# Kernel tuning notes

Hardware: AMD Instinct MI355X
Metric: run time of the kernel (lower is better)

## Reference

```python
import jax, jax.numpy as jnp
import numpy as np

PIANO_SAMPLES = 2_621_440          # multiple of 256 (~119 s @ 22050 Hz)
BLOCK = 512
HOP = 256
N_STEPS = PIANO_SAMPLES // HOP      # 10240 loop iterations
N_FRAMES = PIANO_SAMPLES // HOP + 2 # 10242
UPSAMPLE = 256 // 32                # 8, as in F.upsample(scale_factor=8)


def _hamming(n=BLOCK):
    # torch.hamming_window default: periodic=True
    return (0.54 - 0.46 * jnp.cos(2.0 * jnp.pi * jnp.arange(n, dtype=jnp.float32) / n)).astype(jnp.float32)


def _upsample_linear(v, scale):
    # F.upsample(mode='linear', align_corners=False) on a 1D signal
    n = v.shape[0]
    coords = (jnp.arange(n * scale, dtype=jnp.float32) + 0.5) / scale - 0.5
    coords = jnp.clip(coords, 0.0, n - 1.0)
    lo = jnp.floor(coords).astype(jnp.int32)
    hi = jnp.minimum(lo + 1, n - 1)
    w = coords - lo.astype(jnp.float32)
    return v[lo] * (1.0 - w) + v[hi] * w


def setup_inputs() -> dict:
    key = jax.random.key(0)
    k1, k2, k3, k4, k5, k6 = jax.random.split(key, 6)
    return {
        "x": jnp.zeros((1,), jnp.float32),  # unused by the original forward
        "excitation_env": jax.random.uniform(k1, (N_FRAMES * 32,), jnp.float32) * 0.01,
        "tf_real": jax.random.uniform(k2, (N_FRAMES, 257), jnp.float32) * 0.2,
        "tf_imag": jax.random.uniform(k3, (N_FRAMES, 257), jnp.float32) * 0.2,
        "etf_real": jax.random.uniform(k4, (257,), jnp.float32) * 0.2,
        "etf_imag": jax.random.uniform(k5, (257,), jnp.float32) * 0.2,
        # per-step uniform(-1,1) noise (torch draws this inside forward)
        "noise": jax.random.uniform(k6, (N_STEPS, BLOCK), jnp.float32) * 2.0 - 1.0,
    }


def reference(x, excitation_env, tf_real, tf_imag, etf_real, etf_imag, noise):
    tf = (tf_real + 1j * tf_imag).astype(jnp.complex64)      # [N_FRAMES, 257]
    etf = (etf_real + 1j * etf_imag).astype(jnp.complex64)   # [257]
    win = _hamming()

    # excitation envelope: square then linear-upsample x8 -> len PIANO_SAMPLES + 512
    exc = _upsample_linear(excitation_env ** 2, UPSAMPLE)

    # gather all 512-sample excitation windows at hop 256 -> [N_STEPS, 512]
    idx = jnp.arange(N_STEPS)[:, None] * HOP + jnp.arange(BLOCK)[None, :]
    exc_blocks = exc[idx]

    # batched excitation filtering (independent per step -> fully vectorized)
    imp = noise * exc_blocks
    imp = jnp.fft.irfft(jnp.fft.rfft(imp, norm='ortho') * etf, norm='ortho').astype(jnp.float32)

    # impulse added to the *previous* block at steps 1..N_STEPS-1; last block gets none
    imp_next = jnp.concatenate([imp[1:], jnp.zeros((1, BLOCK), imp.dtype)], axis=0)

    def step(s, inp):
        tf_i, inext = inp
        b = win * jnp.fft.irfft(jnp.fft.rfft(s, norm='ortho') * tf_i, norm='ortho').astype(jnp.float32)
        s_next = b + inext
        return s_next, s_next

    s0 = imp[0]  # learned_impulse=False -> first block is the filtered excitation
    _, ys = jax.lax.scan(step, s0, (tf[:N_STEPS], imp_next))

    blocks = jnp.concatenate([s0[None, :], ys], axis=0)  # [N_STEPS+1, 512]

    # overlap-add with hop 256
    n_b = blocks.shape[0]
    out = jnp.zeros((n_b * HOP + (BLOCK - HOP),), blocks.dtype)
    oa_idx = jnp.arange(n_b)[:, None] * HOP + jnp.arange(BLOCK)[None, :]
    out = out.at[oa_idx].add(blocks)
    return out[:PIANO_SAMPLES]
```

## Files before the change

kernel.cpp:

```cpp
#include <hip/hip_runtime.h>
#include <math.h>

#define N_STEPS 10240
#define ROWF2 264
#define ROWF  (ROWF2*2)
#define ENV_N 327744
#define LCH 16
#define KWARM 16

typedef float f4 __attribute__((ext_vector_type(4)));

__device__ inline float2 mkf2(float x, float y) { return make_float2(x, y); }

template<int DIR>
__device__ inline void waveFFT256(float2 v[4], const int l,
                                  const float Tc, const float Ts,
                                  const float ux, const float uy) {
  const int rb = (int)(__brev((unsigned)l) >> 26);
  #pragma unroll
  for (int r = 0; r < 4; ++r) {
    v[r].x = __shfl(v[r].x, rb);
    v[r].y = __shfl(v[r].y, rb);
  }
  #pragma unroll
  for (int s = 0; s < 6; ++s) {
    const int half = 1 << s;
    float wx, wy;
    if (s == 0) { wx = (l & 1) ? -1.f : 1.f; wy = 0.f; }
    else {
      const int idx = (l << (5 - s)) & 63;
      wx = __shfl(Tc, idx);
      float tsv = __shfl(Ts, idx);
      wy = (DIR < 0) ? tsv : -tsv;
    }
    #pragma unroll
    for (int r = 0; r < 4; ++r) {
      float tx = __shfl_xor(v[r].x, half);
      float ty = __shfl_xor(v[r].y, half);
      const bool low = (l & half) == 0;
      float ax = low ? v[r].x : tx, ay = low ? v[r].y : ty;
      float bx = low ? tx : v[r].x, by = low ? ty : v[r].y;
      v[r].x = ax + (wx * bx - wy * by);
      v[r].y = ay + (wx * by + wy * bx);
    }
  }
  const float u2x = ux * ux - uy * uy, u2y = 2.f * ux * uy;
  const float u3x = u2x * ux - u2y * uy, u3y = u2x * uy + u2y * ux;
  float2 t0 = v[0];
  float2 t1 = mkf2(v[1].x * ux - v[1].y * uy, v[1].x * uy + v[1].y * ux);
  float2 t2 = mkf2(v[2].x * u2x - v[2].y * u2y, v[2].x * u2y + v[2].y * u2x);
  float2 t3 = mkf2(v[3].x * u3x - v[3].y * u3y, v[3].x * u3y + v[3].y * u3x);
  float2 p02 = mkf2(t0.x + t2.x, t0.y + t2.y), m02 = mkf2(t0.x - t2.x, t0.y - t2.y);
  float2 p13 = mkf2(t1.x + t3.x, t1.y + t3.y), m13 = mkf2(t1.x - t3.x, t1.y - t3.y);
  v[0] = mkf2(p02.x + p13.x, p02.y + p13.y);
  v[2] = mkf2(p02.x - p13.x, p02.y - p13.y);
  if (DIR < 0) {
    v[1] = mkf2(m02.x + m13.y, m02.y - m13.x);
    v[3] = mkf2(m02.x - m13.y, m02.y + m13.x);
  } else {
    v[1] = mkf2(m02.x - m13.y, m02.y + m13.x);
    v[3] = mkf2(m02.x + m13.y, m02.y - m13.x);
  }
}

__global__ __launch_bounds__(256) void kernA(const float* __restrict__ env,
                                             const float* __restrict__ noise,
                                             const float* __restrict__ tf_re,
                                             const float* __restrict__ etf_re,
                                             const float* __restrict__ etf_im,
                                             float* __restrict__ IMP,
                                             float* __restrict__ T256,
                                             float* __restrict__ I256) {
  const int l = threadIdx.x & 63;
  const int j = blockIdx.x * 4 + (threadIdx.x >> 6);
  float* rowf = IMP + (size_t)j * ROWF;
  float2* row = (float2*)rowf;
  if (j >= N_STEPS) {
    if (j == N_STEPS) {
      #pragma unroll
      for (int r = 0; r < 4; ++r) row[64 * r + l] = mkf2(0.f, 0.f);
      if (l == 0) { row[256] = mkf2(0.f, 0.f); I256[N_STEPS] = 0.f; }
    }
    return;
  }
  const int K = 32 * j + l;
  float e0 = env[K];                e0 *= e0;
  float em = env[max(K - 1, 0)];    em *= em;
  float ep = env[min(K + 1, ENV_N - 1)]; ep *= ep;
  float sm[8];
  #pragma unroll
  for (int u = 0; u < 8; ++u) {
    float val;
    if (u < 4) {
      float fr = 0.5625f + 0.125f * (float)u;
      val = em * (1.f - fr) + e0 * fr;
      if (K == 0) val = e0;
    } else {
      float fr = 0.0625f + 0.125f * (float)(u - 4);
      val = e0 * (1.f - fr) + ep * fr;
    }
    sm[u] = val;
  }
  const float4* np = (const float4*)(noise + (size_t)j * 512 + 8 * l);
  float4 n0 = np[0], n1 = np[1];
  float nn[8] = {n0.x, n0.y, n0.z, n0.w, n1.x, n1.y, n1.z, n1.w};
  float2 v[4];
  #pragma unroll
  for (int r = 0; r < 4; ++r)
    v[r] = mkf2(nn[2 * r] * sm[2 * r], nn[2 * r + 1] * sm[2 * r + 1]);

  float ca, sa; sincosf(-0.01227184630308513f * (float)l, &sa, &ca);
  const float ux = ca * ca - sa * sa, uy = 2.f * ca * sa;
  float Tc, Ts; sincosf(-0.09817477042468103f * (float)l, &Ts, &Tc);

  waveFFT256<-1>(v, l, Tc, Ts, ux, uy);

  float2 Zc[4];
  const int pidx = (64 - l) & 63;
  #pragma unroll
  for (int r = 0; r < 4; ++r) {
    Zc[r].x = __shfl(v[3 - r].x, pidx);
    Zc[r].y = __shfl(v[3 - r].y, pidx);
  }
  float2 z0lane = v[0];
  if (l == 0) { Zc[0] = v[0]; Zc[1] = v[3]; Zc[2] = v[2]; Zc[3] = v[1]; }
  constexpr float crA[4] = {1.f, 0.7071067811865476f, 0.f, -0.7071067811865476f};
  constexpr float srA[4] = {0.f, -0.7071067811865476f, -1.f, -0.7071067811865476f};
  const float FS = 0.04419417382415922f;
  #pragma unroll
  for (int r = 0; r < 4; ++r) {
    float Ex = 0.5f * (v[r].x + Zc[r].x), Ey = 0.5f * (v[r].y - Zc[r].y);
    float Dx = v[r].x - Zc[r].x,          Dy = v[r].y + Zc[r].y;
    float Ox = 0.5f * Dy, Oy = -0.5f * Dx;
    float c  = crA[r] * ca - srA[r] * sa;
    float sn = crA[r] * sa + srA[r] * ca;
    float Wx = (Ex + (c * Ox - sn * Oy)) * FS;
    float Wy = (Ey + (c * Oy + sn * Ox)) * FS;
    int k = 64 * r + l;
    float er = etf_re[k], ei = etf_im[k];
    float Px = Wx * er - Wy * ei;
    float Py = Wx * ei + Wy * er;
    if (k == 0) Py = 0.f;
    row[k] = mkf2(Px, Py);
  }
  if (l == 0) {
    float W256 = (z0lane.x - z0lane.y) * FS;
    float imp256 = W256 * etf_re[256];
    row[256] = mkf2(imp256, 0.f);
    I256[j] = imp256;
    T256[j] = tf_re[(size_t)j * 257 + 256];
  }
}

struct Slot { f4 tr, ti, ia, ib; };

__device__ inline void issueSlot(Slot& b, int i, int l,
                                 const float* __restrict__ tf_re,
                                 const float* __restrict__ tf_im,
                                 const float* __restrict__ IMP) {
  const float* atr = tf_re + (size_t)i * 257 + 4 * l;
  const float* ati = tf_im + (size_t)i * 257 + 4 * l;
  const float* aim = IMP + (size_t)(i + 1) * ROWF + 8 * l;
  asm volatile("global_load_dwordx4 %0, %1, off" : "=v"(b.tr) : "v"(atr));
  asm volatile("global_load_dwordx4 %0, %1, off" : "=v"(b.ti) : "v"(ati));
  asm volatile("global_load_dwordx4 %0, %1, off" : "=v"(b.ia) : "v"(aim));
  asm volatile("global_load_dwordx4 %0, %1, off offset:16" : "=v"(b.ib) : "v"(aim));
}

__device__ inline void doStep(const Slot& b, int l, float tfr256, float imp256,
                              float2& s0, float2& s1, float2& s2, float2& s3,
                              float& s256) {
  float2 y0, y1, y2, y3;
  y0.x = s0.x * b.tr[0] - s0.y * b.ti[0];  y0.y = s0.x * b.ti[0] + s0.y * b.tr[0];
  y1.x = s1.x * b.tr[1] - s1.y * b.ti[1];  y1.y = s1.x * b.ti[1] + s1.y * b.tr[1];
  y2.x = s2.x * b.tr[2] - s2.y * b.ti[2];  y2.y = s2.x * b.ti[2] + s2.y * b.tr[2];
  y3.x = s3.x * b.tr[3] - s3.y * b.ti[3];  y3.y = s3.x * b.ti[3] + s3.y * b.tr[3];
  if (l == 0) y0.y = 0.f;
  float Y256 = tfr256 * s256;
  float phx = __shfl_up(y3.x, 1), phy = __shfl_up(y3.y, 1);
  float nlx = __shfl_down(y0.x, 1), nly = __shfl_down(y0.y, 1);
  float2 p0 = (l == 0)  ? mkf2(y1.x, -y1.y) : mkf2(phx, phy);
  float2 n3 = (l == 63) ? mkf2(Y256, 0.f)   : mkf2(nlx, nly);
  float y255x = __shfl(y3.x, 63);
  const float A = 0.54f, Bc = 0.23f;
  float2 c0, c1, c2, c3;
  c0.x = A * y0.x - Bc * (p0.x + y1.x);  c0.y = A * y0.y - Bc * (p0.y + y1.y);
  c1.x = A * y1.x - Bc * (y0.x + y2.x);  c1.y = A * y1.y - Bc * (y0.y + y2.y);
  c2.x = A * y2.x - Bc * (y1.x + y3.x);  c2.y = A * y2.y - Bc * (y1.y + y3.y);
  c3.x = A * y3.x - Bc * (y2.x + n3.x);  c3.y = A * y3.y - Bc * (y2.y + n3.y);
  float C256 = A * Y256 - 0.46f * y255x;
  s0.x = c0.x + b.ia[0];  s0.y = c0.y + b.ia[1];
  s1.x = c1.x + b.ia[2];  s1.y = c1.y + b.ia[3];
  s2.x = c2.x + b.ib[0];  s2.y = c2.y + b.ib[1];
  s3.x = c3.x + b.ib[2];  s3.y = c3.y + b.ib[3];
  s256 = C256 + imp256;
}

__device__ inline void ifftState(float2 v[4],
                                 float2 s0, float2 s1, float2 s2, float2 s3,
                                 float s256, int l,
                                 float clC, float slC, float Tc, float Ts,
                                 float cu, float su) {
  float2 W[4] = {s0, s1, s2, s3};
  float2 Wm[4];
  const int pidx = (64 - l) & 63;
  Wm[0].x = __shfl(W[0].x, pidx);
  Wm[0].y = __shfl(W[0].y, pidx);
  if (l == 0) Wm[0] = mkf2(s256, 0.f);
  Wm[1].x = __shfl_xor(W[3].x, 63);  Wm[1].y = __shfl_xor(W[3].y, 63);
  Wm[2].x = __shfl_xor(W[2].x, 63);  Wm[2].y = __shfl_xor(W[2].y, 63);
  Wm[3].x = __shfl_xor(W[1].x, 63);  Wm[3].y = __shfl_xor(W[1].y, 63);
  constexpr float crC[4] = {1.f, 0.9999247018391445f, 0.9996988186962042f, 0.9993223845883495f};
  constexpr float srC[4] = {0.f, 0.0122715382857199f, 0.0245412285229123f, 0.0368072229413588f};
  #pragma unroll
  for (int rr = 0; rr < 4; ++rr) {
    float Ex = 0.5f * (W[rr].x + Wm[rr].x), Ey = 0.5f * (W[rr].y - Wm[rr].y);
    float Dx = W[rr].x - Wm[rr].x,          Dy = W[rr].y + Wm[rr].y;
    float c  = clC * crC[rr] - slC * srC[rr];
    float sn = clC * srC[rr] + slC * crC[rr];
    float Ox = 0.5f * (c * Dx - sn * Dy);
    float Oy = 0.5f * (c * Dy + sn * Dx);
    v[rr] = mkf2(Ex - Oy, Ey + Ox);
  }
  waveFFT256<+1>(v, l, Tc, Ts, cu, su);
}

__global__ __launch_bounds__(64, 1) void kernBC(const float* __restrict__ tf_re,
                                                const float* __restrict__ tf_im,
                                                const float* __restrict__ IMP,
                                                const float* __restrict__ T256,
                                                const float* __restrict__ I256,
                                                float* __restrict__ out) {
  const int c = blockIdx.x, l = threadIdx.x;
  const int j0 = c * LCH;
  const int jend = j0 + LCH;
  const int w0 = max(0, j0 - KWARM);
  const int last = jend - 1;
  float2* out2 = (float2*)out;
  const float ISC = 0.08838834764831845f;

  float t256v = T256[min(w0 + l, N_STEPS - 1)];
  float i256v = I256[min(w0 + 1 + l, N_STEPS)];

  float cu, su; sincosf(0.02454369260617026f * (float)l, &su, &cu);
  const float clC = cu * cu - su * su, slC = 2.f * cu * su;
  float Tc, Ts; sincosf(-0.09817477042468103f * (float)l, &Ts, &Tc);

  float2 s0 = mkf2(0.f, 0.f), s1 = s0, s2 = s0, s3 = s0;
  float s256 = 0.f;
  float2 pt0 = mkf2(0.f, 0.f), pt1 = pt0;

  if (c == 0) {
    const float4* r4 = (const float4*)IMP;
    float4 a = r4[2 * l], bb = r4[2 * l + 1];
    s0 = mkf2(a.x, a.y);  s1 = mkf2(a.z, a.w);
    s2 = mkf2(bb.x, bb.y); s3 = mkf2(bb.z, bb.w);
    s256 = IMP[512];
    float2 v[4];
    ifftState(v, s0, s1, s2, s3, s256, l, clC, slC, Tc, Ts, cu, su);
    out2[l]      = mkf2(v[0].x * ISC, v[0].y * ISC);
    out2[64 + l] = mkf2(v[1].x * ISC, v[1].y * ISC);
    pt0 = mkf2(v[2].x * ISC, v[2].y * ISC);
    pt1 = mkf2(v[3].x * ISC, v[3].y * ISC);
  }

  asm volatile("" :: "v"(t256v), "v"(i256v));
  asm volatile("s_waitcnt vmcnt(0)" ::: "memory");

  Slot b0, b1, b2, b3, b4, b5, b6, b7;
  issueSlot(b0, w0 + 0, l, tf_re, tf_im, IMP);
  issueSlot(b1, w0 + 1, l, tf_re, tf_im, IMP);
  issueSlot(b2, w0 + 2, l, tf_re, tf_im, IMP);
  issueSlot(b3, w0 + 3, l, tf_re, tf_im, IMP);
  issueSlot(b4, w0 + 4, l, tf_re, tf_im, IMP);
  issueSlot(b5, w0 + 5, l, tf_re, tf_im, IMP);
  issueSlot(b6, w0 + 6, l, tf_re, tf_im, IMP);
  issueSlot(b7, w0 + 7, l, tf_re, tf_im, IMP);

  const int rlo   = (c == 0) ? 1 : (j0 - 1);
  const int remit = (c == 0) ? 1 : j0;
  int i = w0;
  #define STEP8(BUF) { \
    asm volatile("s_waitcnt vmcnt(28)" ::: "memory"); \
    __builtin_amdgcn_sched_barrier(0); \
    const int m = i - w0; \
    const float tfr_ = __shfl(t256v, m); \
    const float im2_ = __shfl(i256v, m); \
    doStep(BUF, l, tfr_, im2_, s0, s1, s2, s3, s256); \
    const int r = i + 1; \
    if (r >= rlo && r < jend) { \
      float2 v[4]; \
      ifftState(v, s0, s1, s2, s3, s256, l, clC, slC, Tc, Ts, cu, su); \
      if (r >= remit) { \
        out2[(size_t)r * 128 + l]      = mkf2(v[0].x * ISC + pt0.x, v[0].y * ISC + pt0.y); \
        out2[(size_t)r * 128 + 64 + l] = mkf2(v[1].x * ISC + pt1.x, v[1].y * ISC + pt1.y); \
      } \
      pt0 = mkf2(v[2].x * ISC, v[2].y * ISC); \
      pt1 = mkf2(v[3].x * ISC, v[3].y * ISC); \
    } \
    int nx = i + 8; nx = (nx > last) ? last : nx; \
    issueSlot(BUF, nx, l, tf_re, tf_im, IMP); \
    ++i; }
  while (i < jend) {
    STEP8(b0) STEP8(b1) STEP8(b2) STEP8(b3)
    STEP8(b4) STEP8(b5) STEP8(b6) STEP8(b7)
  }
  #undef STEP8
}

extern "C" void kernel_launch(void* const* d_in, const int* in_sizes, int n_in,
                              void* d_out, int out_size, void* d_ws, size_t ws_size,
                              hipStream_t stream) {
  const float* env    = (const float*)d_in[1];
  const float* tf_re  = (const float*)d_in[2];
  const float* tf_im  = (const float*)d_in[3];
  const float* etf_re = (const float*)d_in[4];
  const float* etf_im = (const float*)d_in[5];
  const float* noise  = (const float*)d_in[6];
  float* out = (float*)d_out;

  float* wsf = (float*)d_ws;
  float* IMP  = wsf;
  float* T256 = wsf + (size_t)(N_STEPS + 1) * ROWF;
  float* I256 = T256 + N_STEPS;

  kernA<<<(N_STEPS / 4) + 1, 256, 0, stream>>>(env, noise, tf_re, etf_re, etf_im,
                                               IMP, T256, I256);
  kernBC<<<N_STEPS / LCH, 64, 0, stream>>>(tf_re, tf_im, IMP, T256, I256, out);
}
```

Baseline: 58.81 us.

## Split recurrence and inverse FFT into separate kernels with LDS-staged states

The fused recurrence kernel is split in two. kernB now only advances the frequency-domain state, stages each step's state in LDS and writes it to a workspace buffer. A new kernC runs the inverse FFT and overlap-add for 8 blocks per 576-thread workgroup. This takes the per-step inverse FFT off the serial critical path of the 64-thread recurrence waves and spreads it across many more waves, at the cost of an extra kernel launch and a round trip of about 21 MB of state through global memory.

```diff
diff --git a/kernel.cpp b/kernel.cpp
--- a/kernel.cpp
+++ b/kernel.cpp
@@ -4,6 +4,7 @@
 #define N_STEPS 10240
 #define ROWF2 264
 #define ROWF  (ROWF2*2)
+#define SROWF 512
 #define ENV_N 327744
 #define LCH 16
 #define KWARM 16
@@ -196,59 +197,25 @@
   s256 = C256 + imp256;
 }
 
-__device__ inline void ifftState(float2 v[4],
-                                 float2 s0, float2 s1, float2 s2, float2 s3,
-                                 float s256, int l,
-                                 float clC, float slC, float Tc, float Ts,
-                                 float cu, float su) {
-  float2 W[4] = {s0, s1, s2, s3};
-  float2 Wm[4];
-  const int pidx = (64 - l) & 63;
-  Wm[0].x = __shfl(W[0].x, pidx);
-  Wm[0].y = __shfl(W[0].y, pidx);
-  if (l == 0) Wm[0] = mkf2(s256, 0.f);
-  Wm[1].x = __shfl_xor(W[3].x, 63);  Wm[1].y = __shfl_xor(W[3].y, 63);
-  Wm[2].x = __shfl_xor(W[2].x, 63);  Wm[2].y = __shfl_xor(W[2].y, 63);
-  Wm[3].x = __shfl_xor(W[1].x, 63);  Wm[3].y = __shfl_xor(W[1].y, 63);
-  constexpr float crC[4] = {1.f, 0.9999247018391445f, 0.9996988186962042f, 0.9993223845883495f};
-  constexpr float srC[4] = {0.f, 0.0122715382857199f, 0.0245412285229123f, 0.0368072229413588f};
-  #pragma unroll
-  for (int rr = 0; rr < 4; ++rr) {
-    float Ex = 0.5f * (W[rr].x + Wm[rr].x), Ey = 0.5f * (W[rr].y - Wm[rr].y);
-    float Dx = W[rr].x - Wm[rr].x,          Dy = W[rr].y + Wm[rr].y;
-    float c  = clC * crC[rr] - slC * srC[rr];
-    float sn = clC * srC[rr] + slC * crC[rr];
-    float Ox = 0.5f * (c * Dx - sn * Dy);
-    float Oy = 0.5f * (c * Dy + sn * Dx);
-    v[rr] = mkf2(Ex - Oy, Ey + Ox);
-  }
-  waveFFT256<+1>(v, l, Tc, Ts, cu, su);
-}
-
-__global__ __launch_bounds__(64, 1) void kernBC(const float* __restrict__ tf_re,
-                                                const float* __restrict__ tf_im,
-                                                const float* __restrict__ IMP,
-                                                const float* __restrict__ T256,
-                                                const float* __restrict__ I256,
-                                                float* __restrict__ out) {
+__global__ __launch_bounds__(64, 1) void kernB(const float* __restrict__ tf_re,
+                                               const float* __restrict__ tf_im,
+                                               const float* __restrict__ IMP,
+                                               const float* __restrict__ T256,
+                                               const float* __restrict__ I256,
+                                               float* __restrict__ S,
+                                               float* __restrict__ S256a) {
   const int c = blockIdx.x, l = threadIdx.x;
   const int j0 = c * LCH;
-  const int jend = j0 + LCH;
-  const int w0 = max(0, j0 - KWARM);
-  const int last = jend - 1;
-  float2* out2 = (float2*)out;
-  const float ISC = 0.08838834764831845f;
+  const int w0 = (c > 0) ? (j0 - KWARM) : 0;
+  const int WOFF = (c > 0) ? KWARM : 0;
+
+  __shared__ float Ssh[LCH * SROWF];
 
   float t256v = T256[min(w0 + l, N_STEPS - 1)];
   float i256v = I256[min(w0 + 1 + l, N_STEPS)];
 
-  float cu, su; sincosf(0.02454369260617026f * (float)l, &su, &cu);
-  const float clC = cu * cu - su * su, slC = 2.f * cu * su;
-  float Tc, Ts; sincosf(-0.09817477042468103f * (float)l, &Ts, &Tc);
-
   float2 s0 = mkf2(0.f, 0.f), s1 = s0, s2 = s0, s3 = s0;
-  float s256 = 0.f;
-  float2 pt0 = mkf2(0.f, 0.f), pt1 = pt0;
+  float s256 = 0.f, s256keep = 0.f;
 
   if (c == 0) {
     const float4* r4 = (const float4*)IMP;
@@ -256,12 +223,9 @@
     s0 = mkf2(a.x, a.y);  s1 = mkf2(a.z, a.w);
     s2 = mkf2(bb.x, bb.y); s3 = mkf2(bb.z, bb.w);
     s256 = IMP[512];
-    float2 v[4];
-    ifftState(v, s0, s1, s2, s3, s256, l, clC, slC, Tc, Ts, cu, su);
-    out2[l]      = mkf2(v[0].x * ISC, v[0].y * ISC);
-    out2[64 + l] = mkf2(v[1].x * ISC, v[1].y * ISC);
-    pt0 = mkf2(v[2].x * ISC, v[2].y * ISC);
-    pt1 = mkf2(v[3].x * ISC, v[3].y * ISC);
+    float4* o4 = (float4*)S;
+    o4[2 * l] = a; o4[2 * l + 1] = bb;
+    if (l == 0) S256a[0] = s256;
   }
 
   asm volatile("" :: "v"(t256v), "v"(i256v));
@@ -277,35 +241,122 @@
   issueSlot(b6, w0 + 6, l, tf_re, tf_im, IMP);
   issueSlot(b7, w0 + 7, l, tf_re, tf_im, IMP);
 
-  const int rlo   = (c == 0) ? 1 : (j0 - 1);
-  const int remit = (c == 0) ? 1 : j0;
-  int i = w0;
-  #define STEP8(BUF) { \
-    asm volatile("s_waitcnt vmcnt(28)" ::: "memory"); \
-    __builtin_amdgcn_sched_barrier(0); \
-    const int m = i - w0; \
-    const float tfr_ = __shfl(t256v, m); \
-    const float im2_ = __shfl(i256v, m); \
+  #define WAITN(NSTR) \
+    asm volatile("s_waitcnt vmcnt(" NSTR ")" ::: "memory"); \
+    __builtin_amdgcn_sched_barrier(0);
+
+  #define WARMSTEP(BUF, M) { \
+    WAITN("28") \
+    const float tfr_ = __shfl(t256v, M); \
+    const float im2_ = __shfl(i256v, M); \
     doStep(BUF, l, tfr_, im2_, s0, s1, s2, s3, s256); \
-    const int r = i + 1; \
-    if (r >= rlo && r < jend) { \
-      float2 v[4]; \
-      ifftState(v, s0, s1, s2, s3, s256, l, clC, slC, Tc, Ts, cu, su); \
-      if (r >= remit) { \
-        out2[(size_t)r * 128 + l]      = mkf2(v[0].x * ISC + pt0.x, v[0].y * ISC + pt0.y); \
-        out2[(size_t)r * 128 + 64 + l] = mkf2(v[1].x * ISC + pt1.x, v[1].y * ISC + pt1.y); \
-      } \
-      pt0 = mkf2(v[2].x * ISC, v[2].y * ISC); \
-      pt1 = mkf2(v[3].x * ISC, v[3].y * ISC); \
-    } \
-    int nx = i + 8; nx = (nx > last) ? last : nx; \
-    issueSlot(BUF, nx, l, tf_re, tf_im, IMP); \
-    ++i; }
-  while (i < jend) {
-    STEP8(b0) STEP8(b1) STEP8(b2) STEP8(b3)
-    STEP8(b4) STEP8(b5) STEP8(b6) STEP8(b7)
-  }
-  #undef STEP8
+    issueSlot(BUF, w0 + (M) + 8, l, tf_re, tf_im, IMP); }
+
+  #define SAVE_LDS(K) { \
+    float4* d4 = (float4*)(Ssh + (K) * SROWF + 8 * l); \
+    d4[0] = make_float4(s0.x, s0.y, s1.x, s1.y); \
+    d4[1] = make_float4(s2.x, s2.y, s3.x, s3.y); \
+    if (l == (K)) s256keep = s256; }
+
+  #define MAINSTEP(BUF, K) { \
+    WAITN("28") \
+    const float tfr_ = __shfl(t256v, WOFF + (K)); \
+    const float im2_ = __shfl(i256v, WOFF + (K)); \
+    doStep(BUF, l, tfr_, im2_, s0, s1, s2, s3, s256); \
+    SAVE_LDS(K) \
+    issueSlot(BUF, j0 + (K) + 8, l, tf_re, tf_im, IMP); }
+
+  #define MAINSTEPL(BUF, K, NSTR) { \
+    WAITN(NSTR) \
+    const float tfr_ = __shfl(t256v, WOFF + (K)); \
+    const float im2_ = __shfl(i256v, WOFF + (K)); \
+    doStep(BUF, l, tfr_, im2_, s0, s1, s2, s3, s256); \
+    SAVE_LDS(K) }
+
+  if (c > 0) {
+    WARMSTEP(b0, 0)  WARMSTEP(b1, 1)  WARMSTEP(b2, 2)  WARMSTEP(b3, 3)
+    WARMSTEP(b4, 4)  WARMSTEP(b5, 5)  WARMSTEP(b6, 6)  WARMSTEP(b7, 7)
+    WARMSTEP(b0, 8)  WARMSTEP(b1, 9)  WARMSTEP(b2, 10) WARMSTEP(b3, 11)
+    WARMSTEP(b4, 12) WARMSTEP(b5, 13) WARMSTEP(b6, 14) WARMSTEP(b7, 15)
+  }
+
+  MAINSTEP(b0, 0)  MAINSTEP(b1, 1)  MAINSTEP(b2, 2)  MAINSTEP(b3, 3)
+  MAINSTEP(b4, 4)  MAINSTEP(b5, 5)  MAINSTEP(b6, 6)  MAINSTEP(b7, 7)
+  MAINSTEPL(b0, 8,  "28") MAINSTEPL(b1, 9,  "24")
+  MAINSTEPL(b2, 10, "20") MAINSTEPL(b3, 11, "16")
+  MAINSTEPL(b4, 12, "12") MAINSTEPL(b5, 13, "8")
+  MAINSTEPL(b6, 14, "4")  MAINSTEPL(b7, 15, "0")
+
+  #undef WAITN
+  #undef WARMSTEP
+  #undef SAVE_LDS
+  #undef MAINSTEP
+  #undef MAINSTEPL
+
+  for (int K = 0; K < LCH; ++K) {
+    const float4* i4 = (const float4*)(Ssh + K * SROWF + 8 * l);
+    float4* o4 = (float4*)(S + (size_t)(j0 + 1 + K) * SROWF + 8 * l);
+    o4[0] = i4[0];
+    o4[1] = i4[1];
+  }
+  if (l < LCH) S256a[j0 + 1 + l] = s256keep;
+}
+
+__global__ __launch_bounds__(576) void kernC(const float* __restrict__ S,
+                                             const float* __restrict__ S256a,
+                                             float* __restrict__ out) {
+  const int l = threadIdx.x & 63;
+  const int w = threadIdx.x >> 6;
+  const int b = blockIdx.x;
+  const int r = 8 * b - 1 + w;
+  __shared__ float2 ybuf[9][256];
+  if (r < 0) {
+    #pragma unroll
+    for (int rr = 0; rr < 4; ++rr) ybuf[0][64 * rr + l] = mkf2(0.f, 0.f);
+  } else {
+    const float4* r4 = (const float4*)(S + (size_t)r * SROWF);
+    float4 a = r4[2 * l], bb = r4[2 * l + 1];
+    float2 W[4] = {mkf2(a.x, a.y), mkf2(a.z, a.w), mkf2(bb.x, bb.y), mkf2(bb.z, bb.w)};
+    float w256 = S256a[r];
+    float2 Wm[4];
+    const int pidx = (64 - l) & 63;
+    Wm[0].x = __shfl(W[0].x, pidx);
+    Wm[0].y = __shfl(W[0].y, pidx);
+    if (l == 0) Wm[0] = mkf2(w256, 0.f);
+    Wm[1].x = __shfl_xor(W[3].x, 63);  Wm[1].y = __shfl_xor(W[3].y, 63);
+    Wm[2].x = __shfl_xor(W[2].x, 63);  Wm[2].y = __shfl_xor(W[2].y, 63);
+    Wm[3].x = __shfl_xor(W[1].x, 63);  Wm[3].y = __shfl_xor(W[1].y, 63);
+    float cu, su; sincosf(0.02454369260617026f * (float)l, &su, &cu);
+    const float cl = cu * cu - su * su, sl_ = 2.f * cu * su;
+    float Tc, Ts; sincosf(-0.09817477042468103f * (float)l, &Ts, &Tc);
+    constexpr float crC[4] = {1.f, 0.9999247018391445f, 0.9996988186962042f, 0.9993223845883495f};
+    constexpr float srC[4] = {0.f, 0.0122715382857199f, 0.0245412285229123f, 0.0368072229413588f};
+    float2 v[4];
+    #pragma unroll
+    for (int rr = 0; rr < 4; ++rr) {
+      float Ex = 0.5f * (W[rr].x + Wm[rr].x), Ey = 0.5f * (W[rr].y - Wm[rr].y);
+      float Dx = W[rr].x - Wm[rr].x,          Dy = W[rr].y + Wm[rr].y;
+      float c  = cl * crC[rr] - sl_ * srC[rr];
+      float sn = cl * srC[rr] + sl_ * crC[rr];
+      float Ox = 0.5f * (c * Dx - sn * Dy);
+      float Oy = 0.5f * (c * Dy + sn * Dx);
+      v[rr] = mkf2(Ex - Oy, Ey + Ox);
+    }
+    waveFFT256<+1>(v, l, Tc, Ts, cu, su);
+    const float ISC = 0.08838834764831845f;
+    #pragma unroll
+    for (int rr = 0; rr < 4; ++rr)
+      ybuf[w][64 * rr + l] = mkf2(v[rr].x * ISC, v[rr].y * ISC);
+  }
+  __syncthreads();
+  float2* out2 = (float2*)out;
+  const size_t base = (size_t)b * 1024;
+  for (int idx = threadIdx.x; idx < 1024; idx += 576) {
+    const int k = idx >> 7, t2 = idx & 127;
+    float2 a = ybuf[k + 1][t2];
+    float2 p = ybuf[k][128 + t2];
+    out2[base + idx] = mkf2(a.x + p.x, a.y + p.y);
+  }
 }
 
 extern "C" void kernel_launch(void* const* d_in, const int* in_sizes, int n_in,
@@ -320,11 +371,14 @@
   float* out = (float*)d_out;
 
   float* wsf = (float*)d_ws;
-  float* IMP  = wsf;
-  float* T256 = wsf + (size_t)(N_STEPS + 1) * ROWF;
-  float* I256 = T256 + N_STEPS;
+  float* IMP   = wsf;
+  float* S     = wsf + (size_t)(N_STEPS + 1) * ROWF;
+  float* T256  = S + (size_t)(N_STEPS + 1) * SROWF;
+  float* I256  = T256 + N_STEPS;
+  float* S256a = I256 + (N_STEPS + 1);
 
   kernA<<<(N_STEPS / 4) + 1, 256, 0, stream>>>(env, noise, tf_re, etf_re, etf_im,
                                                IMP, T256, I256);
-  kernBC<<<N_STEPS / LCH, 64, 0, stream>>>(tf_re, tf_im, IMP, T256, I256, out);
-}
+  kernB<<<N_STEPS / LCH, 64, 0, stream>>>(tf_re, tf_im, IMP, T256, I256, S, S256a);
+  kernC<<<N_STEPS / 8, 576, 0, stream>>>(S, S256a, out);
+}
```

Result: faster. 54.83 us (-6.8%).
